# Kernel tuning notes

Hardware: AMD Instinct MI355X
Metric: run time of the kernel (lower is better)

Reference implementation:

```python
import jax, jax.numpy as jnp
import numpy as np

H = 16
D_MODEL = 1024
D_HEAD = D_MODEL // H  # 64


def _xavier(key, shape):
    # xavier_uniform over last two dims (matches torch init on [h, in, out])
    fan_in, fan_out = shape[-2], shape[-1]
    limit = float(np.sqrt(6.0 / (fan_in + fan_out)))
    return jax.random.uniform(key, shape, jnp.float32, -limit, limit)


def setup_inputs() -> dict:
    key = jax.random.key(0)
    ks = jax.random.split(key, 7)
    B, S = 4, 2048
    x_q = jax.random.normal(ks[0], (B, S, D_MODEL), jnp.float32)
    x_k = jax.random.normal(ks[1], (B, S, D_MODEL), jnp.float32)
    x_v = jax.random.normal(ks[2], (B, S, D_MODEL), jnp.float32)
    W_Q = _xavier(ks[3], (H, D_MODEL, D_HEAD))
    W_K = _xavier(ks[4], (H, D_MODEL, D_HEAD))
    W_V = _xavier(ks[5], (H, D_MODEL, D_HEAD))
    # torch Linear weight: [out_features, in_features], y = x @ W^T
    lim = float(np.sqrt(6.0 / (2 * D_MODEL)))  # kaiming-uniform-ish default approximated by xavier for reproducibility
    W_O = jax.random.uniform(ks[6], (D_MODEL, D_MODEL), jnp.float32, -lim, lim)
    return {"x_q": x_q, "x_k": x_k, "x_v": x_v,
            "W_Q": W_Q, "W_K": W_K, "W_V": W_V, "W_O": W_O}


def reference(x_q, x_k, x_v, W_Q, W_K, W_V, W_O):
    d_scale = jnp.asarray(D_HEAD, jnp.float32) ** 0.25  # d_q == d_k == dim_q**(1/4)
    # per-head projections: [b,s,m] x [h,m,d] -> [b,h,s,d]
    Q = jnp.einsum('bsm,hmd->bhsd', x_q, W_Q)
    K = jnp.einsum('bsm,hmd->bhsd', x_k, W_K)
    V = jnp.einsum('bsm,hmd->bhsd', x_v, W_V)
    # column softmax over K^T: shape [b,h,d,s], softmax over dim=-2 (the d axis)
    Kt = jnp.swapaxes(K, -1, -2) / d_scale          # [b,h,d,s]
    Kt = jax.nn.softmax(Kt, axis=-2)
    A = jnp.einsum('bhds,bhse->bhde', Kt, V)        # KV precompute [b,h,d,d]
    Qs = jax.nn.softmax(Q / d_scale, axis=-1)       # row softmax over head dim
    Bt = jnp.einsum('bhsd,bhde->bhse', Qs, A)       # [b,h,s,d]
    b, h, s, d = Bt.shape
    # faithful to torch .view on contiguous [b,h,s,d] -> [b,s,h*d] (pure reshape, no transpose)
    Bt = Bt.reshape(b, s, h * d)
    return jnp.einsum('bsi,oi->bso', Bt, W_O)
```

## Files before the change

### kernel.cpp

```cpp
#include <hip/hip_runtime.h>
#include <cstdint>
#include <cstddef>

#define DMODEL 1024
#define HEADS  16
#define DHEAD  64
#define BATCH  4
#define SEQ    2048
#define ROWS   (BATCH * SEQ)
#define INV_DSCALE 0.3535533905932738f

typedef float  f32x4  __attribute__((ext_vector_type(4)));
typedef __bf16 bf16x8 __attribute__((ext_vector_type(8)));
typedef unsigned short u16x8 __attribute__((ext_vector_type(8)));

__device__ __forceinline__ unsigned short f2bf(float x) {
    union { float f; unsigned u; } c; c.f = x;
    unsigned u = c.u;
    return (unsigned short)((u + 0x7fffu + ((u >> 16) & 1u)) >> 16);
}

__device__ __forceinline__ unsigned cvt_pk_bf16(float a, float b) {
#if __has_builtin(__builtin_amdgcn_cvt_pk_bf16_f32)
    typedef __bf16 bf16x2_t __attribute__((ext_vector_type(2)));
    union { bf16x2_t v; unsigned u; } c;
    c.v = __builtin_amdgcn_cvt_pk_bf16_f32(a, b);
    return c.u;
#else
    return (unsigned)f2bf(a) | ((unsigned)f2bf(b) << 16);
#endif
}

__device__ __forceinline__ void load_g2l16(const unsigned short* g, unsigned short* l) {
    __builtin_amdgcn_global_load_lds(
        (const __attribute__((address_space(1))) unsigned int*)g,
        (__attribute__((address_space(3))) unsigned int*)l,
        16 , 0 , 0 );
}

__global__ __launch_bounds__(256) void prep_w(const float* __restrict__ W0,
                                              const float* __restrict__ W1,
                                              const float* __restrict__ W2,
                                              const float* __restrict__ Wo,
                                              const float* __restrict__ Xq,
                                              const float* __restrict__ Xk,
                                              const float* __restrict__ Xv,
                                              unsigned short* __restrict__ T0,
                                              unsigned short* __restrict__ T1,
                                              unsigned short* __restrict__ T2,
                                              unsigned short* __restrict__ To,
                                              unsigned short* __restrict__ Xb) {
    __shared__ float tile[64][68];
    int blk = blockIdx.x;
    int t = threadIdx.x;
    if (blk < 768) {
        int w = blk >> 8, h = (blk >> 4) & 15, mb = blk & 15;
        const float* W = w == 0 ? W0 : (w == 1 ? W1 : W2);
        unsigned short* T = w == 0 ? T0 : (w == 1 ? T1 : T2);
        #pragma unroll
        for (int i = 0; i < 4; ++i) {
            int f = t + 256 * i;
            int m = f >> 4, dg = (f & 15) * 4;
            *(float4*)&tile[m][dg] = *(const float4*)&W[((size_t)(h * 16 + mb) * 64 + m) * 64 + dg];
        }
        __syncthreads();
        #pragma unroll
        for (int i = 0; i < 2; ++i) {
            int f = t + 256 * i;
            int d = f >> 3, mg = f & 7;
            ushort4 a, b;
            a.x = f2bf(tile[mg * 8 + 0][d]); a.y = f2bf(tile[mg * 8 + 1][d]);
            a.z = f2bf(tile[mg * 8 + 2][d]); a.w = f2bf(tile[mg * 8 + 3][d]);
            b.x = f2bf(tile[mg * 8 + 4][d]); b.y = f2bf(tile[mg * 8 + 5][d]);
            b.z = f2bf(tile[mg * 8 + 6][d]); b.w = f2bf(tile[mg * 8 + 7][d]);
            unsigned short* dst = T + (size_t)(h * 64 + d) * DMODEL + mb * 64 + mg * 8;
            *(ushort4*)dst = a; *(ushort4*)(dst + 4) = b;
        }
    } else if (blk < 1792) {
        int i = (blk - 768) * 256 + t;
        float4 v = ((const float4*)Wo)[i];
        ushort4 o;
        o.x = f2bf(v.x); o.y = f2bf(v.y); o.z = f2bf(v.z); o.w = f2bf(v.w);
        ((ushort4*)To)[i] = o;
    } else {
        int bb = blk - 1792;
        int w = bb >> 12;
        int i = (bb & 4095) * 256 + t;
        const float* X = w == 0 ? Xq : (w == 1 ? Xk : Xv);
        const float4* src = (const float4*)X + (size_t)i * 2;
        float4 a = src[0], b = src[1];
        uint4 pk;
        pk.x = cvt_pk_bf16(a.x, a.y);
        pk.y = cvt_pk_bf16(a.z, a.w);
        pk.z = cvt_pk_bf16(b.x, b.y);
        pk.w = cvt_pk_bf16(b.z, b.w);
        ((uint4*)(Xb + (size_t)w * ROWS * DMODEL))[i] = pk;
    }
}

__device__ __forceinline__ void gemm_tile(const unsigned short* __restrict__ Ap,
                                          const unsigned short* __restrict__ Bp,
                                          int K, int bm0, int bn0,
                                          unsigned short* smem, f32x4 acc[4][4]) {
    unsigned short* ldsA = smem;
    unsigned short* ldsB = smem + 8192;

    const int t    = threadIdx.x;
    const int lane = t & 63;
    const int wave = t >> 6;
    const int wm   = (wave & 1) * 64;
    const int wn   = (wave >> 1) * 64;
    const int fr   = lane & 15;
    const int quad = lane >> 4;

    unsigned offA[4], offB[4];
    #pragma unroll
    for (int i = 0; i < 4; ++i) {
        int f = t + 256 * i, row = f >> 3, kg = (f & 7) ^ (row & 7);
        offA[i] = (unsigned)(bm0 + row) * K + kg * 8;
        offB[i] = (unsigned)(bn0 + row) * K + kg * 8;
    }

    for (int k0 = 0; k0 < K; k0 += 64) {
        #pragma unroll
        for (int i = 0; i < 4; ++i)
            load_g2l16(Ap + offA[i] + k0, &ldsA[(t + 256 * i) * 8]);
        #pragma unroll
        for (int i = 0; i < 4; ++i)
            load_g2l16(Bp + offB[i] + k0, &ldsB[(t + 256 * i) * 8]);
        asm volatile("s_waitcnt vmcnt(0)" ::: "memory");
        __syncthreads();

        bf16x8 af[4][2], bfr[4][2];
        #pragma unroll
        for (int i = 0; i < 4; ++i) {
            int row = wm + i * 16 + fr;
            #pragma unroll
            for (int kh = 0; kh < 2; ++kh) {
                int s = (kh * 4 + quad) ^ (row & 7);
                af[i][kh] = *reinterpret_cast<const bf16x8*>(&ldsA[row * 64 + s * 8]);
            }
        }
        #pragma unroll
        for (int j = 0; j < 4; ++j) {
            int row = wn + j * 16 + fr;
            #pragma unroll
            for (int kh = 0; kh < 2; ++kh) {
                int s = (kh * 4 + quad) ^ (row & 7);
                bfr[j][kh] = *reinterpret_cast<const bf16x8*>(&ldsB[row * 64 + s * 8]);
            }
        }
        #pragma unroll
        for (int kh = 0; kh < 2; ++kh)
            #pragma unroll
            for (int i = 0; i < 4; ++i)
                #pragma unroll
                for (int j = 0; j < 4; ++j)
                    acc[i][j] = __builtin_amdgcn_mfma_f32_16x16x32_bf16(af[i][kh], bfr[j][kh], acc[i][j], 0, 0, 0);

        __syncthreads();
    }
}

__device__ __forceinline__ void softmax4(float v[4]) {
    #pragma unroll
    for (int j = 0; j < 4; ++j) v[j] *= INV_DSCALE;
    float m = fmaxf(fmaxf(v[0], v[1]), fmaxf(v[2], v[3]));
    #pragma unroll
    for (int off = 8; off; off >>= 1) m = fmaxf(m, __shfl_xor(m, off, 16));
    float s = 0.f;
    #pragma unroll
    for (int j = 0; j < 4; ++j) { v[j] = __expf(v[j] - m); s += v[j]; }
    #pragma unroll
    for (int off = 8; off; off >>= 1) s += __shfl_xor(s, off, 16);
    float inv = 1.0f / s;
    #pragma unroll
    for (int j = 0; j < 4; ++j) v[j] *= inv;
}

__device__ __forceinline__ void decode_blk(int flat, int& bm0, int& bn0) {
    int xcd = flat & 7, idx = flat >> 3;
    bm0 = (xcd * 8 + (idx >> 3)) * 128;
    bn0 = (idx & 7) * 128;
}

__global__ __launch_bounds__(256, 2) void proj3(const unsigned short* __restrict__ Xb,
                                                const unsigned short* __restrict__ wq,
                                                const unsigned short* __restrict__ wk,
                                                const unsigned short* __restrict__ wv,
                                                unsigned short* __restrict__ Qb,
                                                unsigned short* __restrict__ Kt,
                                                unsigned short* __restrict__ Vt) {
    __shared__ unsigned short smem[17408];
    int z = blockIdx.y;
    const unsigned short* A = Xb + (size_t)z * ROWS * DMODEL;
    const unsigned short* B = z == 0 ? wq : (z == 1 ? wk : wv);
    int bm0, bn0;
    decode_blk(blockIdx.x, bm0, bn0);

    f32x4 acc[4][4] = {};
    gemm_tile(A, B, DMODEL, bm0, bn0, smem, acc);

    const int t    = threadIdx.x;
    const int lane = t & 63;
    const int wave = t >> 6;
    const int wm   = (wave & 1) * 64;
    const int wn   = (wave >> 1) * 64;
    const int fr   = lane & 15;
    const int quad = lane >> 4;
    bool do_sm = (z < 2);

    if (z == 0) {
        #pragma unroll
        for (int i = 0; i < 4; ++i)
            #pragma unroll
            for (int r = 0; r < 4; ++r) {
                float v[4];
                #pragma unroll
                for (int j = 0; j < 4; ++j) v[j] = acc[i][j][r];
                softmax4(v);
                int rr = bm0 + wm + i * 16 + quad * 4 + r;
                size_t base = (size_t)rr * DMODEL + bn0 + wn + fr;
                #pragma unroll
                for (int j = 0; j < 4; ++j) Qb[base + j * 16] = f2bf(v[j]);
            }
    } else {
        unsigned short* Ct = smem;
        #pragma unroll
        for (int i = 0; i < 4; ++i)
            #pragma unroll
            for (int r = 0; r < 4; ++r) {
                float v[4];
                #pragma unroll
                for (int j = 0; j < 4; ++j) v[j] = acc[i][j][r];
                if (do_sm) softmax4(v);
                int rr = wm + i * 16 + quad * 4 + r;
                #pragma unroll
                for (int j = 0; j < 4; ++j) {
                    int cc = wn + j * 16 + fr;
                    Ct[cc * 136 + rr] = f2bf(v[j]);
                }
            }
        __syncthreads();
        unsigned short* T = (z == 1) ? Kt : Vt;
        int c = t >> 1, sh = (t & 1) * 64;
        int col = bn0 + c, h = col >> 6, d = col & 63;
        int b = bm0 >> 11, s0 = bm0 & 2047;
        unsigned short* dst = T + (((size_t)(b * 16 + h) * 64 + d) << 11) + s0 + sh;
        const unsigned short* src = &smem[c * 136 + sh];
        #pragma unroll
        for (int k = 0; k < 8; ++k)
            *(uint4*)(dst + k * 8) = *(const uint4*)(src + k * 8);
    }
}

__global__ __launch_bounds__(256, 2) void gemm_out(const unsigned short* __restrict__ R,
                                                   const unsigned short* __restrict__ Wo,
                                                   float* __restrict__ out) {
    __shared__ unsigned short smem[16384];
    int bm0, bn0;
    decode_blk(blockIdx.x, bm0, bn0);
    f32x4 acc[4][4] = {};
    gemm_tile(R, Wo, DMODEL, bm0, bn0, smem, acc);

    const int t = threadIdx.x, lane = t & 63, wave = t >> 6;
    const int wm = (wave & 1) * 64, wn = (wave >> 1) * 64;
    const int fr = lane & 15, quad = lane >> 4;
    #pragma unroll
    for (int i = 0; i < 4; ++i)
        #pragma unroll
        for (int r = 0; r < 4; ++r) {
            int rr = bm0 + wm + i * 16 + quad * 4 + r;
            size_t base = (size_t)rr * DMODEL + bn0 + wn + fr;
            #pragma unroll
            for (int j = 0; j < 4; ++j) out[base + j * 16] = acc[i][j][r];
        }
}

__global__ __launch_bounds__(256) void kv_mfma(const unsigned short* __restrict__ Vt,
                                               const unsigned short* __restrict__ Kt,
                                               float* __restrict__ P) {
    __shared__ unsigned short ldsV[64 * 64];
    __shared__ unsigned short ldsK[64 * 64];
    int bh = blockIdx.x >> 3, chunk = blockIdx.x & 7;
    int t = threadIdx.x, lane = t & 63, wave = t >> 6;
    int fr = lane & 15, quad = lane >> 4;

    unsigned offV[2], offK[2];
    #pragma unroll
    for (int i = 0; i < 2; ++i) {
        int f = t + 256 * i, row = f >> 3, kg = (f & 7) ^ (row & 7);
        unsigned o = ((unsigned)(bh * 64 + row) << 11) + chunk * 256 + kg * 8;
        offV[i] = o; offK[i] = o;
    }

    f32x4 acc[4] = {};
    for (int k0 = 0; k0 < 256; k0 += 64) {
        #pragma unroll
        for (int i = 0; i < 2; ++i)
            load_g2l16(Vt + offV[i] + k0, &ldsV[(t + 256 * i) * 8]);
        #pragma unroll
        for (int i = 0; i < 2; ++i)
            load_g2l16(Kt + offK[i] + k0, &ldsK[(t + 256 * i) * 8]);
        asm volatile("s_waitcnt vmcnt(0)" ::: "memory");
        __syncthreads();

        #pragma unroll
        for (int kh = 0; kh < 2; ++kh) {
            int rowA = wave * 16 + fr;
            int sA = (kh * 4 + quad) ^ (rowA & 7);
            bf16x8 av = *reinterpret_cast<const bf16x8*>(&ldsV[rowA * 64 + sA * 8]);
            #pragma unroll
            for (int j = 0; j < 4; ++j) {
                int rowB = j * 16 + fr;
                int sB = (kh * 4 + quad) ^ (rowB & 7);
                bf16x8 bv = *reinterpret_cast<const bf16x8*>(&ldsK[rowB * 64 + sB * 8]);
                acc[j] = __builtin_amdgcn_mfma_f32_16x16x32_bf16(av, bv, acc[j], 0, 0, 0);
            }
        }
        __syncthreads();
    }
    float* Pp = P + ((size_t)chunk * 64 + bh) * 4096;
    #pragma unroll
    for (int j = 0; j < 4; ++j)
        #pragma unroll
        for (int r = 0; r < 4; ++r)
            Pp[(wave * 16 + quad * 4 + r) * 64 + j * 16 + fr] = acc[j][r];
}

__global__ __launch_bounds__(256) void reduce_A(const float* __restrict__ P,
                                                unsigned short* __restrict__ At) {
    int idx = blockIdx.x * 256 + threadIdx.x;
    float s = 0.f;
    #pragma unroll
    for (int c = 0; c < 8; ++c) s += P[(size_t)c * (64 * 4096) + idx];
    At[idx] = f2bf(s);
}

__global__ __launch_bounds__(256, 4) void qs_mfma(const unsigned short* __restrict__ Qb,
                                                  const unsigned short* __restrict__ At,
                                                  unsigned short* __restrict__ R) {
    __shared__ unsigned short ldsQ[128 * 64];
    __shared__ unsigned short ldsB[64 * 64];
    int bh = blockIdx.x >> 4, sb = blockIdx.x & 15;
    int b = bh >> 4, h = bh & 15;
    int t = threadIdx.x, lane = t & 63, wave = t >> 6;
    int fr = lane & 15, quad = lane >> 4;
    int wm = wave * 32;

    #pragma unroll
    for (int i = 0; i < 4; ++i) {
        int f = t + 256 * i, row = f >> 3, kg = (f & 7) ^ (row & 7);
        const unsigned short* src = Qb + ((size_t)(b * SEQ + sb * 128 + row) << 10) + h * 64 + kg * 8;
        load_g2l16(src, &ldsQ[f * 8]);
    }
    #pragma unroll
    for (int i = 0; i < 2; ++i) {
        int f = t + 256 * i, row = f >> 3, kg = (f & 7) ^ (row & 7);
        load_g2l16(At + (unsigned)bh * 4096 + row * 64 + kg * 8, &ldsB[f * 8]);
    }
    asm volatile("s_waitcnt vmcnt(0)" ::: "memory");
    __syncthreads();

    f32x4 acc[2][4] = {};
    #pragma unroll
    for (int kh = 0; kh < 2; ++kh) {
        bf16x8 af[2], bfr[4];
        #pragma unroll
        for (int i = 0; i < 2; ++i) {
            int row = wm + i * 16 + fr;
            int s = (kh * 4 + quad) ^ (row & 7);
            af[i] = *reinterpret_cast<const bf16x8*>(&ldsQ[row * 64 + s * 8]);
        }
        #pragma unroll
        for (int j = 0; j < 4; ++j) {
            int row = j * 16 + fr;
            int s = (kh * 4 + quad) ^ (row & 7);
            bfr[j] = *reinterpret_cast<const bf16x8*>(&ldsB[row * 64 + s * 8]);
        }
        #pragma unroll
        for (int i = 0; i < 2; ++i)
            #pragma unroll
            for (int j = 0; j < 4; ++j)
                acc[i][j] = __builtin_amdgcn_mfma_f32_16x16x32_bf16(af[i], bfr[j], acc[i][j], 0, 0, 0);
    }

    #pragma unroll
    for (int i = 0; i < 2; ++i)
        #pragma unroll
        for (int r = 0; r < 4; ++r) {
            int rr = wm + i * 16 + quad * 4 + r;
            size_t base = ((size_t)bh << 17) + (size_t)(sb * 128 + rr) * 64;
            #pragma unroll
            for (int j = 0; j < 4; ++j)
                R[base + j * 16 + fr] = f2bf(acc[i][j][r]);
        }
}

extern "C" void kernel_launch(void* const* d_in, const int* in_sizes, int n_in,
                              void* d_out, int out_size, void* d_ws, size_t ws_size,
                              hipStream_t stream) {
    const float* xq = (const float*)d_in[0];
    const float* xk = (const float*)d_in[1];
    const float* xv = (const float*)d_in[2];
    const float* Wq = (const float*)d_in[3];
    const float* Wk = (const float*)d_in[4];
    const float* Wv = (const float*)d_in[5];
    const float* Wo = (const float*)d_in[6];
    float* out = (float*)d_out;
    char* ws = (char*)d_ws;

    const size_t MB = 1ull << 20;
    unsigned short* wq_t = (unsigned short*)(ws + 0 * MB);
    unsigned short* wk_t = (unsigned short*)(ws + 2 * MB);
    unsigned short* wv_t = (unsigned short*)(ws + 4 * MB);
    unsigned short* wo_b = (unsigned short*)(ws + 6 * MB);
    unsigned short* Qb = (unsigned short*)(ws + 8 * MB);
    unsigned short* Kt = (unsigned short*)(ws + 24 * MB);
    unsigned short* Vt = (unsigned short*)(ws + 40 * MB);
    unsigned short* At = (unsigned short*)(ws + 56 * MB);
    unsigned short* Xb = (unsigned short*)(ws + 57 * MB);
    unsigned short* R  = (unsigned short*)(ws + 57 * MB);
    float* P = (float*)(ws + 73 * MB);

    prep_w<<<14080, 256, 0, stream>>>(Wq, Wk, Wv, Wo, xq, xk, xv,
                                      wq_t, wk_t, wv_t, wo_b, Xb);

    proj3<<<dim3(512, 3), 256, 0, stream>>>(Xb, wq_t, wk_t, wv_t, Qb, Kt, Vt);

    kv_mfma<<<BATCH * HEADS * 8, 256, 0, stream>>>(Vt, Kt, P);
    reduce_A<<<1024, 256, 0, stream>>>(P, At);

    qs_mfma<<<BATCH * HEADS * 16, 256, 0, stream>>>(Qb, At, R);

    gemm_out<<<512, 256, 0, stream>>>(R, wo_b, out);
}
```

Measured before the change: 262.2 us.

## Fuse Q projection with softmax and Qs·A product into one kernel

Moves the Q projection to after the KV reduction, so the projected tile is softmaxed into LDS and immediately multiplied by the per-head A matrices loaded alongside. This removes the Qb intermediate write and read and the separate qs_mfma launch. The X conversion blocks now each process two chunks, which halves the prep grid, and the workspace layout is reorganised to match. In exchange proj_q uses more LDS (48KB), which could lower occupancy, and the Q GEMM now sits on the serial dependency chain after reduce_A.

```diff
diff --git a/kernel.cpp b/kernel.cpp
--- a/kernel.cpp
+++ b/kernel.cpp
@@ -12,7 +12,6 @@
 
 typedef float  f32x4  __attribute__((ext_vector_type(4)));
 typedef __bf16 bf16x8 __attribute__((ext_vector_type(8)));
-typedef unsigned short u16x8 __attribute__((ext_vector_type(8)));
 
 __device__ __forceinline__ unsigned short f2bf(float x) {
     union { float f; unsigned u; } c; c.f = x;
@@ -84,17 +83,22 @@
         ((ushort4*)To)[i] = o;
     } else {
         int bb = blk - 1792;
-        int w = bb >> 12;
-        int i = (bb & 4095) * 256 + t;
+        int w = bb >> 11;
+        int g0 = (bb & 2047) * 256 + t;
         const float* X = w == 0 ? Xq : (w == 1 ? Xk : Xv);
-        const float4* src = (const float4*)X + (size_t)i * 2;
-        float4 a = src[0], b = src[1];
-        uint4 pk;
-        pk.x = cvt_pk_bf16(a.x, a.y);
-        pk.y = cvt_pk_bf16(a.z, a.w);
-        pk.z = cvt_pk_bf16(b.x, b.y);
-        pk.w = cvt_pk_bf16(b.z, b.w);
-        ((uint4*)(Xb + (size_t)w * ROWS * DMODEL))[i] = pk;
+        unsigned short* D = Xb + (size_t)w * ROWS * DMODEL;
+        #pragma unroll
+        for (int u = 0; u < 2; ++u) {
+            size_t g = (size_t)g0 + (size_t)u * 524288;
+            const float4* src = (const float4*)X + g * 2;
+            float4 a = src[0], bv = src[1];
+            uint4 pk;
+            pk.x = cvt_pk_bf16(a.x, a.y);
+            pk.y = cvt_pk_bf16(a.z, a.w);
+            pk.z = cvt_pk_bf16(bv.x, bv.y);
+            pk.w = cvt_pk_bf16(bv.z, bv.w);
+            ((uint4*)D)[g] = pk;
+        }
     }
 }
 
@@ -184,17 +188,15 @@
     bn0 = (idx & 7) * 128;
 }
 
-__global__ __launch_bounds__(256, 2) void proj3(const unsigned short* __restrict__ Xb,
-                                                const unsigned short* __restrict__ wq,
-                                                const unsigned short* __restrict__ wk,
-                                                const unsigned short* __restrict__ wv,
-                                                unsigned short* __restrict__ Qb,
-                                                unsigned short* __restrict__ Kt,
-                                                unsigned short* __restrict__ Vt) {
+__global__ __launch_bounds__(256, 2) void proj_kv(const unsigned short* __restrict__ Xb,
+                                                  const unsigned short* __restrict__ wk,
+                                                  const unsigned short* __restrict__ wv,
+                                                  unsigned short* __restrict__ Kt,
+                                                  unsigned short* __restrict__ Vt) {
     __shared__ unsigned short smem[17408];
-    int z = blockIdx.y;
+    int z = blockIdx.y + 1;
     const unsigned short* A = Xb + (size_t)z * ROWS * DMODEL;
-    const unsigned short* B = z == 0 ? wq : (z == 1 ? wk : wv);
+    const unsigned short* B = (z == 1) ? wk : wv;
     int bm0, bn0;
     decode_blk(blockIdx.x, bm0, bn0);
 
@@ -208,50 +210,119 @@
     const int wn   = (wave >> 1) * 64;
     const int fr   = lane & 15;
     const int quad = lane >> 4;
-    bool do_sm = (z < 2);
-
-    if (z == 0) {
+    bool do_sm = (z == 1);
+
+    unsigned short* Ct = smem;
+    #pragma unroll
+    for (int i = 0; i < 4; ++i)
+        #pragma unroll
+        for (int r = 0; r < 4; ++r) {
+            float v[4];
+            #pragma unroll
+            for (int j = 0; j < 4; ++j) v[j] = acc[i][j][r];
+            if (do_sm) softmax4(v);
+            int rr = wm + i * 16 + quad * 4 + r;
+            #pragma unroll
+            for (int j = 0; j < 4; ++j) {
+                int cc = wn + j * 16 + fr;
+                Ct[cc * 136 + rr] = f2bf(v[j]);
+            }
+        }
+    __syncthreads();
+    unsigned short* T = (z == 1) ? Kt : Vt;
+    int c = t >> 1, sh = (t & 1) * 64;
+    int col = bn0 + c, h = col >> 6, d = col & 63;
+    int b = bm0 >> 11, s0 = bm0 & 2047;
+    unsigned short* dst = T + (((size_t)(b * 16 + h) * 64 + d) << 11) + s0 + sh;
+    const unsigned short* src = &smem[c * 136 + sh];
+    #pragma unroll
+    for (int k = 0; k < 8; ++k)
+        *(uint4*)(dst + k * 8) = *(const uint4*)(src + k * 8);
+}
+
+__global__ __launch_bounds__(256, 2) void proj_q(const unsigned short* __restrict__ Xb,
+                                                 const unsigned short* __restrict__ wq,
+                                                 const unsigned short* __restrict__ At,
+                                                 unsigned short* __restrict__ R) {
+    __shared__ unsigned short smem[24576];
+    int bm0, bn0;
+    decode_blk(blockIdx.x, bm0, bn0);
+
+    f32x4 acc[4][4] = {};
+    gemm_tile(Xb, wq, DMODEL, bm0, bn0, smem, acc);
+
+    const int t = threadIdx.x, lane = t & 63, wave = t >> 6;
+    const int wm = (wave & 1) * 64, wn = (wave >> 1) * 64;
+    const int fr = lane & 15, quad = lane >> 4;
+    const int b = bm0 >> 11, s0 = bm0 & 2047;
+    const int h0 = bn0 >> 6;
+    const int bh_base = b * 16 + h0;
+
+    unsigned short* Qs = smem;
+    unsigned short* ldsAt = smem + 16384;
+
+    #pragma unroll
+    for (int i = 0; i < 4; ++i) {
+        int f = t + 256 * i;
+        int hd = f >> 9, row = (f >> 3) & 63, kg = (f & 7) ^ (row & 7);
+        load_g2l16(At + (size_t)(bh_base + hd) * 4096 + row * 64 + kg * 8,
+                   &ldsAt[f * 8]);
+    }
+
+    #pragma unroll
+    for (int i = 0; i < 4; ++i)
+        #pragma unroll
+        for (int r = 0; r < 4; ++r) {
+            float v[4];
+            #pragma unroll
+            for (int j = 0; j < 4; ++j) v[j] = acc[i][j][r];
+            softmax4(v);
+            int row = wm + i * 16 + quad * 4 + r;
+            #pragma unroll
+            for (int j = 0; j < 4; ++j) {
+                int c = wn + j * 16 + fr;
+                int cs = (c & 0x47) | (((((c >> 3) & 7) ^ (row & 7))) << 3);
+                Qs[row * 128 + cs] = f2bf(v[j]);
+            }
+        }
+    asm volatile("s_waitcnt vmcnt(0)" ::: "memory");
+    __syncthreads();
+
+    const int hw = wn >> 6;
+    f32x4 racc[4][4] = {};
+    #pragma unroll
+    for (int kh = 0; kh < 2; ++kh) {
+        bf16x8 aq[4], bt[4];
+        #pragma unroll
+        for (int i = 0; i < 4; ++i) {
+            int row = wm + i * 16 + fr;
+            int s = (kh * 4 + quad) ^ (row & 7);
+            aq[i] = *reinterpret_cast<const bf16x8*>(&Qs[row * 128 + wn + s * 8]);
+        }
+        #pragma unroll
+        for (int j = 0; j < 4; ++j) {
+            int e = j * 16 + fr;
+            int s = (kh * 4 + quad) ^ (e & 7);
+            bt[j] = *reinterpret_cast<const bf16x8*>(&ldsAt[(hw << 12) + e * 64 + s * 8]);
+        }
         #pragma unroll
         for (int i = 0; i < 4; ++i)
             #pragma unroll
-            for (int r = 0; r < 4; ++r) {
-                float v[4];
-                #pragma unroll
-                for (int j = 0; j < 4; ++j) v[j] = acc[i][j][r];
-                softmax4(v);
-                int rr = bm0 + wm + i * 16 + quad * 4 + r;
-                size_t base = (size_t)rr * DMODEL + bn0 + wn + fr;
-                #pragma unroll
-                for (int j = 0; j < 4; ++j) Qb[base + j * 16] = f2bf(v[j]);
-            }
-    } else {
-        unsigned short* Ct = smem;
-        #pragma unroll
-        for (int i = 0; i < 4; ++i)
-            #pragma unroll
-            for (int r = 0; r < 4; ++r) {
-                float v[4];
-                #pragma unroll
-                for (int j = 0; j < 4; ++j) v[j] = acc[i][j][r];
-                if (do_sm) softmax4(v);
-                int rr = wm + i * 16 + quad * 4 + r;
-                #pragma unroll
-                for (int j = 0; j < 4; ++j) {
-                    int cc = wn + j * 16 + fr;
-                    Ct[cc * 136 + rr] = f2bf(v[j]);
-                }
-            }
-        __syncthreads();
-        unsigned short* T = (z == 1) ? Kt : Vt;
-        int c = t >> 1, sh = (t & 1) * 64;
-        int col = bn0 + c, h = col >> 6, d = col & 63;
-        int b = bm0 >> 11, s0 = bm0 & 2047;
-        unsigned short* dst = T + (((size_t)(b * 16 + h) * 64 + d) << 11) + s0 + sh;
-        const unsigned short* src = &smem[c * 136 + sh];
-        #pragma unroll
-        for (int k = 0; k < 8; ++k)
-            *(uint4*)(dst + k * 8) = *(const uint4*)(src + k * 8);
-    }
+            for (int j = 0; j < 4; ++j)
+                racc[i][j] = __builtin_amdgcn_mfma_f32_16x16x32_bf16(aq[i], bt[j], racc[i][j], 0, 0, 0);
+    }
+
+    size_t bh = (size_t)(bh_base + hw);
+    #pragma unroll
+    for (int i = 0; i < 4; ++i)
+        #pragma unroll
+        for (int r = 0; r < 4; ++r) {
+            int rr = wm + i * 16 + quad * 4 + r;
+            size_t base = (bh << 17) + (size_t)(s0 + rr) * 64;
+            #pragma unroll
+            for (int j = 0; j < 4; ++j)
+                R[base + j * 16 + fr] = f2bf(racc[i][j][r]);
+        }
 }
 
 __global__ __launch_bounds__(256, 2) void gemm_out(const unsigned short* __restrict__ R,
@@ -335,66 +406,6 @@
     #pragma unroll
     for (int c = 0; c < 8; ++c) s += P[(size_t)c * (64 * 4096) + idx];
     At[idx] = f2bf(s);
-}
-
-__global__ __launch_bounds__(256, 4) void qs_mfma(const unsigned short* __restrict__ Qb,
-                                                  const unsigned short* __restrict__ At,
-                                                  unsigned short* __restrict__ R) {
-    __shared__ unsigned short ldsQ[128 * 64];
-    __shared__ unsigned short ldsB[64 * 64];
-    int bh = blockIdx.x >> 4, sb = blockIdx.x & 15;
-    int b = bh >> 4, h = bh & 15;
-    int t = threadIdx.x, lane = t & 63, wave = t >> 6;
-    int fr = lane & 15, quad = lane >> 4;
-    int wm = wave * 32;
-
-    #pragma unroll
-    for (int i = 0; i < 4; ++i) {
-        int f = t + 256 * i, row = f >> 3, kg = (f & 7) ^ (row & 7);
-        const unsigned short* src = Qb + ((size_t)(b * SEQ + sb * 128 + row) << 10) + h * 64 + kg * 8;
-        load_g2l16(src, &ldsQ[f * 8]);
-    }
-    #pragma unroll
-    for (int i = 0; i < 2; ++i) {
-        int f = t + 256 * i, row = f >> 3, kg = (f & 7) ^ (row & 7);
-        load_g2l16(At + (unsigned)bh * 4096 + row * 64 + kg * 8, &ldsB[f * 8]);
-    }
-    asm volatile("s_waitcnt vmcnt(0)" ::: "memory");
-    __syncthreads();
-
-    f32x4 acc[2][4] = {};
-    #pragma unroll
-    for (int kh = 0; kh < 2; ++kh) {
-        bf16x8 af[2], bfr[4];
-        #pragma unroll
-        for (int i = 0; i < 2; ++i) {
-            int row = wm + i * 16 + fr;
-            int s = (kh * 4 + quad) ^ (row & 7);
-            af[i] = *reinterpret_cast<const bf16x8*>(&ldsQ[row * 64 + s * 8]);
-        }
-        #pragma unroll
-        for (int j = 0; j < 4; ++j) {
-            int row = j * 16 + fr;
-            int s = (kh * 4 + quad) ^ (row & 7);
-            bfr[j] = *reinterpret_cast<const bf16x8*>(&ldsB[row * 64 + s * 8]);
-        }
-        #pragma unroll
-        for (int i = 0; i < 2; ++i)
-            #pragma unroll
-            for (int j = 0; j < 4; ++j)
-                acc[i][j] = __builtin_amdgcn_mfma_f32_16x16x32_bf16(af[i], bfr[j], acc[i][j], 0, 0, 0);
-    }
-
-    #pragma unroll
-    for (int i = 0; i < 2; ++i)
-        #pragma unroll
-        for (int r = 0; r < 4; ++r) {
-            int rr = wm + i * 16 + quad * 4 + r;
-            size_t base = ((size_t)bh << 17) + (size_t)(sb * 128 + rr) * 64;
-            #pragma unroll
-            for (int j = 0; j < 4; ++j)
-                R[base + j * 16 + fr] = f2bf(acc[i][j][r]);
-        }
 }
 
 extern "C" void kernel_launch(void* const* d_in, const int* in_sizes, int n_in,
@@ -415,23 +426,22 @@
     unsigned short* wk_t = (unsigned short*)(ws + 2 * MB);
     unsigned short* wv_t = (unsigned short*)(ws + 4 * MB);
     unsigned short* wo_b = (unsigned short*)(ws + 6 * MB);
-    unsigned short* Qb = (unsigned short*)(ws + 8 * MB);
-    unsigned short* Kt = (unsigned short*)(ws + 24 * MB);
-    unsigned short* Vt = (unsigned short*)(ws + 40 * MB);
-    unsigned short* At = (unsigned short*)(ws + 56 * MB);
-    unsigned short* Xb = (unsigned short*)(ws + 57 * MB);
-    unsigned short* R  = (unsigned short*)(ws + 57 * MB);
-    float* P = (float*)(ws + 73 * MB);
-
-    prep_w<<<14080, 256, 0, stream>>>(Wq, Wk, Wv, Wo, xq, xk, xv,
-                                      wq_t, wk_t, wv_t, wo_b, Xb);
-
-    proj3<<<dim3(512, 3), 256, 0, stream>>>(Xb, wq_t, wk_t, wv_t, Qb, Kt, Vt);
+    unsigned short* Xb   = (unsigned short*)(ws + 8 * MB);
+    unsigned short* Kt   = (unsigned short*)(ws + 56 * MB);
+    unsigned short* Vt   = (unsigned short*)(ws + 72 * MB);
+    unsigned short* At   = (unsigned short*)(ws + 88 * MB);
+    float* P            = (float*)(ws + 24 * MB);
+    unsigned short* R   = (unsigned short*)(ws + 40 * MB);
+
+    prep_w<<<7936, 256, 0, stream>>>(Wq, Wk, Wv, Wo, xq, xk, xv,
+                                     wq_t, wk_t, wv_t, wo_b, Xb);
+
+    proj_kv<<<dim3(512, 2), 256, 0, stream>>>(Xb, wk_t, wv_t, Kt, Vt);
 
     kv_mfma<<<BATCH * HEADS * 8, 256, 0, stream>>>(Vt, Kt, P);
     reduce_A<<<1024, 256, 0, stream>>>(P, At);
 
-    qs_mfma<<<BATCH * HEADS * 16, 256, 0, stream>>>(Qb, At, R);
+    proj_q<<<512, 256, 0, stream>>>(Xb, wq_t, At, R);
 
     gemm_out<<<512, 256, 0, stream>>>(R, wo_b, out);
 }
```

Result: no change. 265.8 us (+1.4%).
